# Kernel optimization log

Hardware: AMD Instinct MI355X
Metric: run time of the kernel (lower is better)

Reference implementation:

```python
import jax, jax.numpy as jnp
import numpy as np

N = 4096
D = 256
DEG = 32
E0 = N * DEG
RATIO = 0.5
NEG_SLOPE = 0.2


def setup_inputs() -> dict:
    key = jax.random.key(0)
    ks = jax.random.split(key, 12)
    # edges with NO self loops (so appending all N self-loops == add_remaining_self_loops)
    src = jax.random.randint(ks[0], (E0,), 0, N, dtype=jnp.int32)
    off = jax.random.randint(ks[1], (E0,), 1, N, dtype=jnp.int32)
    dst = ((src + off) % N).astype(jnp.int32)
    edge_index = jnp.stack([src, dst])
    edge_weight = jnp.ones((E0,), jnp.float32)
    x = jax.random.normal(ks[2], (N, D), jnp.float32)
    s = 1.0 / np.sqrt(D)
    u = lambda k, shp: jax.random.uniform(k, shp, jnp.float32, -s, s)
    return {
        'x': x,
        'edge_index': edge_index,
        'edge_weight': edge_weight,
        'lin_w': u(ks[3], (D, D)), 'lin_b': u(ks[4], (D,)),
        'att_w': jax.random.uniform(ks[5], (2 * D, 1), jnp.float32, -1.0 / np.sqrt(2 * D), 1.0 / np.sqrt(2 * D)),
        'att_b': u(ks[6], (1,)),
        'le1_w': u(ks[7], (D, 1)), 'le1_b': u(ks[8], (1,)),
        'le2_w': u(ks[9], (D, 1)),
        'le3_w': u(ks[10], (D, 1)), 'le3_b': u(ks[11], (1,)),
    }


def reference(x, edge_index, edge_weight, lin_w, lin_b, att_w, att_b,
              le1_w, le1_b, le2_w, le3_w, le3_b):
    n, d = x.shape
    # add_remaining_self_loops (input has no self loops by construction)
    loop = jnp.arange(n, dtype=edge_index.dtype)
    src = jnp.concatenate([edge_index[0], loop])
    dst = jnp.concatenate([edge_index[1], loop])
    w = jnp.concatenate([edge_weight, jnp.ones((n,), edge_weight.dtype)])

    # GNN is None -> x_pool = x
    x_pool_j = x[src]                                        # [E, D] gather
    x_q = jax.ops.segment_max(x_pool_j, dst, num_segments=n)  # scatter-max
    x_q_e = (x_q @ lin_w + lin_b)[dst]                        # [E, D]
    # att(cat([x_q, x_pool_j])) without materializing [E, 2D]
    score = x_q_e @ att_w[:d, 0] + x_pool_j @ att_w[d:, 0] + att_b[0]
    score = jax.nn.leaky_relu(score, NEG_SLOPE)
    # segment softmax over destination nodes
    smax = jax.ops.segment_max(score, dst, num_segments=n)
    ex = jnp.exp(score - smax[dst])
    denom = jax.ops.segment_sum(ex, dst, num_segments=n)
    score = ex / denom[dst]
    # dropout p=0 -> no-op
    xn = jax.ops.segment_sum(x_pool_j * score[:, None], dst, num_segments=n)

    # LEConv fitness: sigmoid( lin3(x) + sum_j (lin1(x_j) - lin2(x_i)) )
    a = xn @ le1_w + le1_b          # [N, 1]
    b = xn @ le2_w                  # [N, 1] (no bias)
    agg = jax.ops.segment_sum(a[src] - b[dst], dst, num_segments=n)
    fitness = jax.nn.sigmoid((agg + xn @ le3_w + le3_b)[:, 0])

    k = int(np.ceil(RATIO * N))
    _, perm = jax.lax.top_k(fitness, k)
    x_out = xn[perm] * fitness[perm][:, None]

    # Coarsening A_c = S[:, perm]^T @ A @ S[:, perm]; dense since SpGEMM nnz is data-dependent
    S = jnp.zeros((n, n), x.dtype).at[src, dst].add(score)[:, perm]  # [N, k]
    A = jnp.zeros((n, n), x.dtype).at[src, dst].add(w)               # [N, N]
    A_c = S.T @ (A @ S)                                              # [k, k]
    A_c = A_c * (1.0 - jnp.eye(k, dtype=A_c.dtype))                  # remove_diag
    return x_out, A_c, perm
```

## Files before the change

kernel.cpp:

```cpp
#include <hip/hip_runtime.h>
#include <cstdint>
#include <cstddef>
#include <math.h>

#define NN   4096
#define DD   256
#define E0S  131072
#define NE   (E0S + NN)
#define KK   2048
#define NEG_SLOPE 0.2f
#define SEGCAP 256

typedef float floatx4 __attribute__((ext_vector_type(4)));

__device__ __forceinline__ int esrc(const int* s, int e){ return e < E0S ? s[e] : e - E0S; }
__device__ __forceinline__ int edst(const int* d, int e){ return e < E0S ? d[e] : e - E0S; }

__global__ void init_kernel(int* deg_dst, int* deg_src, int* colmap, float* Ac, int zero_ac){
    int i = blockIdx.x * blockDim.x + threadIdx.x;
    int stride = gridDim.x * blockDim.x;
    if (zero_ac){
        for (size_t t = i; t < (size_t)KK * KK; t += stride) Ac[t] = 0.f;
    }
    for (int t = i; t < NN; t += stride){ deg_dst[t] = 0; deg_src[t] = 0; colmap[t] = -1; }
}

__global__ void count_kernel(const int* e_src, const int* e_dst, int* deg_dst, int* deg_src){
    int e = blockIdx.x * blockDim.x + threadIdx.x;
    if (e < NE){
        atomicAdd(&deg_dst[edst(e_dst, e)], 1);
        atomicAdd(&deg_src[esrc(e_src, e)], 1);
    }
}

__global__ void __launch_bounds__(1024) scan_kernel(const int* degA, int* offA, int* curA,
                                                    const int* degB, int* offB, int* curB){
    const int* deg = (blockIdx.x == 0) ? degA : degB;
    int* off = (blockIdx.x == 0) ? offA : offB;
    int* cur = (blockIdx.x == 0) ? curA : curB;
    __shared__ int part[1024];
    int t = threadIdx.x;
    int base = t * 4;
    int s0 = deg[base], s1 = deg[base+1], s2 = deg[base+2], s3 = deg[base+3];
    int tot = s0 + s1 + s2 + s3;
    part[t] = tot;
    __syncthreads();
    for (int d = 1; d < 1024; d <<= 1){
        int v = (t >= d) ? part[t - d] : 0;
        __syncthreads();
        part[t] += v;
        __syncthreads();
    }
    int excl = part[t] - tot;
    off[base]   = excl;            cur[base]   = excl;
    off[base+1] = excl + s0;       cur[base+1] = excl + s0;
    off[base+2] = excl + s0 + s1;  cur[base+2] = excl + s0 + s1;
    off[base+3] = excl + s0 + s1 + s2; cur[base+3] = excl + s0 + s1 + s2;
    if (t == 1023) off[NN] = part[1023];
}

__global__ void fill_kernel(const int* e_src, const int* e_dst, int* cur_dst, int* cur_src,
                            int* eid_dst, int* eid_src){
    int e = blockIdx.x * blockDim.x + threadIdx.x;
    if (e < NE){
        int p = atomicAdd(&cur_dst[edst(e_dst, e)], 1); eid_dst[p] = e;
        int q = atomicAdd(&cur_src[esrc(e_src, e)], 1); eid_src[q] = e;
    }
}

__global__ void segsort_kernel(const int* off_dst, int* eid_dst, const int* off_src, int* eid_src,
                               const int* e_src, int* isd){
    __shared__ int buf[4][SEGCAP];
    int wid  = (blockIdx.x * blockDim.x + threadIdx.x) >> 6;
    int lane = threadIdx.x & 63;
    int w    = threadIdx.x >> 6;
    const int* off; int* eid; int n; bool isdst;
    if (wid < NN){ off = off_dst; eid = eid_dst; n = wid; isdst = true; }
    else         { off = off_src; eid = eid_src; n = wid - NN; isdst = false; }
    int lo = off[n], hi = off[n+1];
    int L = hi - lo;
    int Lc = (L <= SEGCAP) ? L : SEGCAP;
    for (int i = lane; i < Lc; i += 64) buf[w][i] = eid[lo + i];
    __syncthreads();
    if (L <= SEGCAP){
        for (int i = lane; i < L; i += 64){
            int v = buf[w][i];
            int r = 0;
            for (int j = 0; j < L; ++j) r += (buf[w][j] < v);
            eid[lo + r] = v;
            if (isdst) isd[lo + r] = esrc(e_src, v);
        }
    } else if (lane == 0){
        for (int i = lo + 1; i < hi; ++i){
            int v = eid[i]; int j = i - 1;
            while (j >= lo && eid[j] > v){ eid[j+1] = eid[j]; --j; }
            eid[j+1] = v;
        }
        if (isdst) for (int i = lo; i < hi; ++i) isd[i] = esrc(e_src, eid[i]);
    }
}

__global__ void segmax_kernel(const float* x, const int* off, const int* isd, float* x_q){
    __shared__ int is_[SEGCAP];
    int n = blockIdx.x, d = threadIdx.x;
    int lo = off[n], hi = off[n+1];
    int L = hi - lo;
    int Ls = (L <= SEGCAP) ? L : SEGCAP;
    for (int t = d; t < Ls; t += 256) is_[t] = isd[lo + t];
    __syncthreads();
    float m = -INFINITY;
    int t = 0;
    for (; t + 1 < Ls; t += 2){
        float v0 = x[(size_t)is_[t]   * DD + d];
        float v1 = x[(size_t)is_[t+1] * DD + d];
        m = fmaxf(m, fmaxf(v0, v1));
    }
    if (t < Ls) m = fmaxf(m, x[(size_t)is_[t] * DD + d]);
    for (t = Ls; t < L; ++t)
        m = fmaxf(m, x[(size_t)isd[lo + t] * DD + d]);
    x_q[(size_t)n * DD + d] = m;
}

#define LROWS 8
__global__ void lin_kernel(const float* x_q, const float* w, const float* b, float* out){
    __shared__ float xs[LROWS][DD];
    int col = threadIdx.x;
    int r0 = blockIdx.x * LROWS;
    for (int r = 0; r < LROWS; ++r) xs[r][col] = x_q[(size_t)(r0 + r) * DD + col];
    __syncthreads();
    float acc[LROWS];
    float bc = b[col];
    #pragma unroll
    for (int r = 0; r < LROWS; ++r) acc[r] = bc;
    for (int kk = 0; kk < DD; ++kk){
        float wv = w[(size_t)kk * DD + col];
        #pragma unroll
        for (int r = 0; r < LROWS; ++r) acc[r] = fmaf(xs[r][kk], wv, acc[r]);
    }
    for (int r = 0; r < LROWS; ++r) out[(size_t)(r0 + r) * DD + col] = acc[r];
}

__global__ void nodedots_kernel(const float* x, const float* x_q_lin, const float* att_w,
                                float* q_s, float* p_s){
    int n = blockIdx.x, t = threadIdx.x;
    float v1 = x_q_lin[(size_t)n * DD + t] * att_w[t];
    float v2 = x[(size_t)n * DD + t] * att_w[DD + t];
    __shared__ float s1[256], s2[256];
    s1[t] = v1; s2[t] = v2;
    __syncthreads();
    for (int d = 128; d > 0; d >>= 1){
        if (t < d){ s1[t] += s1[t + d]; s2[t] += s2[t + d]; }
        __syncthreads();
    }
    if (t == 0){ q_s[n] = s1[0]; p_s[n] = s2[0]; }
}

__global__ void softmax_kernel(const int* off, const int* eid, const int* isd,
                               const float* q_s, const float* p_s, const float* att_b,
                               float* sc, float* ssd){
    int wave = threadIdx.x >> 6;
    int lane = threadIdx.x & 63;
    int n = blockIdx.x * 4 + wave;
    int lo = off[n], hi = off[n+1];
    float ab = att_b[0];
    float qn = q_s[n];
    float m = -INFINITY;
    for (int t = lo + lane; t < hi; t += 64){
        float s = qn + p_s[isd[t]] + ab;
        s = (s > 0.f) ? s : NEG_SLOPE * s;
        m = fmaxf(m, s);
    }
    #pragma unroll
    for (int d = 32; d > 0; d >>= 1) m = fmaxf(m, __shfl_xor(m, d));
    float sum = 0.f;
    for (int t = lo + lane; t < hi; t += 64){
        float s = qn + p_s[isd[t]] + ab;
        s = (s > 0.f) ? s : NEG_SLOPE * s;
        float ex = expf(s - m);
        ssd[t] = ex;
        sum += ex;
    }
    #pragma unroll
    for (int d = 32; d > 0; d >>= 1) sum += __shfl_xor(sum, d);
    float inv = 1.f / sum;
    for (int t = lo + lane; t < hi; t += 64){
        float v = ssd[t] * inv;
        ssd[t] = v;
        sc[eid[t]] = v;
    }
}

__global__ void xnfit_kernel(const float* x, const int* off, const int* isd, const float* ssd,
                             const float* le1_w, const float* le1_b, const float* le2_w,
                             const float* le3_w, const float* le3_b,
                             float* xn, float* a_, float* b_, float* c_){
    __shared__ int   is_[SEGCAP];
    __shared__ float ss_[SEGCAP];
    __shared__ float s1[256], s2[256], s3[256];
    int n = blockIdx.x, d = threadIdx.x;
    int lo = off[n], hi = off[n+1];
    int L = hi - lo;
    int Ls = (L <= SEGCAP) ? L : SEGCAP;
    for (int t = d; t < Ls; t += 256){
        is_[t] = isd[lo + t];
        ss_[t] = ssd[lo + t];
    }
    __syncthreads();
    float acc = 0.f;
    int t = 0;
    for (; t + 1 < Ls; t += 2){
        float v0 = x[(size_t)is_[t]   * DD + d];
        float v1 = x[(size_t)is_[t+1] * DD + d];
        acc = fmaf(ss_[t],   v0, acc);
        acc = fmaf(ss_[t+1], v1, acc);
    }
    if (t < Ls) acc = fmaf(ss_[t], x[(size_t)is_[t] * DD + d], acc);
    for (t = Ls; t < L; ++t)
        acc = fmaf(ssd[lo + t], x[(size_t)isd[lo + t] * DD + d], acc);
    xn[(size_t)n * DD + d] = acc;
    s1[d] = acc * le1_w[d];
    s2[d] = acc * le2_w[d];
    s3[d] = acc * le3_w[d];
    __syncthreads();
    for (int dd = 128; dd > 0; dd >>= 1){
        if (d < dd){ s1[d] += s1[d+dd]; s2[d] += s2[d+dd]; s3[d] += s3[d+dd]; }
        __syncthreads();
    }
    if (d == 0){
        a_[n] = s1[0] + le1_b[0];
        b_[n] = s2[0];
        c_[n] = s3[0] + le3_b[0];
    }
}

__global__ void fitness_kernel(const int* off, const int* isd,
                               const float* a_, const float* b_, const float* c_,
                               float* fit){
    int wave = threadIdx.x >> 6;
    int lane = threadIdx.x & 63;
    int n = blockIdx.x * 4 + wave;
    int lo = off[n], hi = off[n+1];
    float bn = b_[n];
    float s = 0.f;
    for (int t = lo + lane; t < hi; t += 64){
        s += a_[isd[t]] - bn;
    }
    #pragma unroll
    for (int d = 32; d > 0; d >>= 1) s += __shfl_xor(s, d);
    if (lane == 0){
        float z = s + c_[n];
        fit[n] = 1.f / (1.f + expf(-z));
    }
}

__global__ void __launch_bounds__(1024) topk_kernel(const float* fit, int* perm, int* colmap,
                                                    float* out_perm){
    __shared__ unsigned long long keys[NN];
    int t = threadIdx.x;
    for (int i = t; i < NN; i += 1024){
        unsigned int u = __float_as_uint(fit[i]);
        u = (u & 0x80000000u) ? ~u : (u | 0x80000000u);
        u = ~u;
        keys[i] = ((unsigned long long)u << 32) | (unsigned int)i;
    }
    __syncthreads();
    for (unsigned int ssize = 2; ssize <= NN; ssize <<= 1){
        for (unsigned int stride = ssize >> 1; stride > 0; stride >>= 1){
            for (int i = t; i < NN / 2; i += 1024){
                unsigned int idx = 2u * i - (i & (stride - 1u));
                unsigned int par = idx + stride;
                bool asc = ((idx & ssize) == 0u);
                unsigned long long a = keys[idx], b = keys[par];
                if ((a > b) == asc){ keys[idx] = b; keys[par] = a; }
            }
            __syncthreads();
        }
    }
    for (int i = t; i < KK; i += 1024){
        int node = (int)(keys[i] & 0xFFFFFFFFull);
        perm[i] = node;
        colmap[node] = i;
        out_perm[i] = (float)node;
    }
}

__global__ void xout_kernel(const float* xn, const float* fit, const int* perm, float* x_out){
    int r = blockIdx.x, d = threadIdx.x;
    int p = perm[r];
    x_out[(size_t)r * DD + d] = xn[(size_t)p * DD + d] * fit[p];
}

__global__ void prepsrc_kernel(const int* eid_src, const int* e_dst, const int* colmap,
                               const float* sc, int* cp, float* sp){
    int u = blockIdx.x * blockDim.x + threadIdx.x;
    if (u < NE){
        int f = eid_src[u];
        cp[u] = colmap[edst(e_dst, f)];
        sp[u] = sc[f];
    }
}

__global__ void spgemm1_kernel(const int* e_dst, const float* ew,
                               const int* off_src, const int* eid_src,
                               const int* cp, const float* sp, float* T){
    __shared__ float row[KK];
    __shared__ int   jlo_[SEGCAP];
    __shared__ int   jhi_[SEGCAP];
    __shared__ float w_[SEGCAP];
    int i = blockIdx.x;
    for (int c = threadIdx.x; c < KK; c += 256) row[c] = 0.f;
    int lo = off_src[i], hi = off_src[i+1];
    int L = hi - lo;
    int Ls = (L <= SEGCAP) ? L : SEGCAP;
    for (int t = threadIdx.x; t < Ls; t += 256){
        int e = eid_src[lo + t];
        int j = edst(e_dst, e);
        jlo_[t] = off_src[j];
        jhi_[t] = off_src[j+1];
        w_[t]   = (e < E0S) ? ew[e] : 1.0f;
    }
    __syncthreads();
    int wave = threadIdx.x >> 6, lane = threadIdx.x & 63;
    for (int t = wave; t < Ls; t += 4){
        float w1 = w_[t];
        for (int u = jlo_[t] + lane; u < jhi_[t]; u += 64){
            int c = cp[u];
            if (c >= 0) atomicAdd(&row[c], w1 * sp[u]);
        }
    }
    for (int t = Ls + wave; t < L; t += 4){
        int e = eid_src[lo + t];
        int j = edst(e_dst, e);
        float w1 = (e < E0S) ? ew[e] : 1.0f;
        int jlo = off_src[j], jhi = off_src[j+1];
        for (int u = jlo + lane; u < jhi; u += 64){
            int c = cp[u];
            if (c >= 0) atomicAdd(&row[c], w1 * sp[u]);
        }
    }
    __syncthreads();
    float* Trow = T + (size_t)i * KK;
    for (int c = threadIdx.x; c < KK; c += 256) Trow[c] = row[c];
}

__global__ void spgemm2_kernel(const int* perm, const int* off_dst,
                               const int* isd, const float* ssd,
                               const float* T, float* Ac){
    __shared__ int   is_[8][SEGCAP];
    __shared__ float ss_[8][SEGCAP];
    int bx = blockIdx.x;
    int by = blockIdx.y;
    int half = by >> 8;
    int rr   = by & 255;
    int sub  = threadIdx.x >> 5;
    int lane = threadIdx.x & 31;
    int r = rr * 8 + sub;
    int chunk = bx + 8 * half;
    int c0 = chunk * 128 + lane * 4;
    int node = perm[r];
    int lo = off_dst[node], hi = off_dst[node+1];
    int L = hi - lo;
    int Ls = (L <= SEGCAP) ? L : SEGCAP;
    for (int t = lane; t < Ls; t += 32){
        is_[sub][t] = isd[lo + t];
        ss_[sub][t] = ssd[lo + t];
    }
    __syncthreads();
    floatx4 acc = {0.f, 0.f, 0.f, 0.f};
    int t = 0;
    for (; t + 1 < Ls; t += 2){
        floatx4 a = *(const floatx4*)&T[(size_t)is_[sub][t]   * KK + c0];
        floatx4 b = *(const floatx4*)&T[(size_t)is_[sub][t+1] * KK + c0];
        float s0 = ss_[sub][t], s1 = ss_[sub][t+1];
        acc.x = fmaf(s0, a.x, acc.x); acc.y = fmaf(s0, a.y, acc.y);
        acc.z = fmaf(s0, a.z, acc.z); acc.w = fmaf(s0, a.w, acc.w);
        acc.x = fmaf(s1, b.x, acc.x); acc.y = fmaf(s1, b.y, acc.y);
        acc.z = fmaf(s1, b.z, acc.z); acc.w = fmaf(s1, b.w, acc.w);
    }
    for (; t < Ls; ++t){
        floatx4 a = *(const floatx4*)&T[(size_t)is_[sub][t] * KK + c0];
        float s0 = ss_[sub][t];
        acc.x = fmaf(s0, a.x, acc.x); acc.y = fmaf(s0, a.y, acc.y);
        acc.z = fmaf(s0, a.z, acc.z); acc.w = fmaf(s0, a.w, acc.w);
    }
    for (t = Ls; t < L; ++t){
        floatx4 a = *(const floatx4*)&T[(size_t)isd[lo + t] * KK + c0];
        float s0 = ssd[lo + t];
        acc.x = fmaf(s0, a.x, acc.x); acc.y = fmaf(s0, a.y, acc.y);
        acc.z = fmaf(s0, a.z, acc.z); acc.w = fmaf(s0, a.w, acc.w);
    }
    if (r - c0 >= 0 && r - c0 < 4){
        if (r - c0 == 0) acc.x = 0.f;
        else if (r - c0 == 1) acc.y = 0.f;
        else if (r - c0 == 2) acc.z = 0.f;
        else acc.w = 0.f;
    }
    __builtin_nontemporal_store(acc, (floatx4*)&Ac[(size_t)r * KK + c0]);
}

__global__ void ac_kernel(const int* e_src, const int* e_dst, const float* ew,
                          const int* off_src,
                          const int* cp, const float* sp, float* Ac){
    int e1 = blockIdx.x * blockDim.x + threadIdx.x;
    if (e1 >= NE) return;
    int i = (e1 < E0S) ? e_src[e1] : e1 - E0S;
    int j = (e1 < E0S) ? e_dst[e1] : e1 - E0S;
    float w1 = (e1 < E0S) ? ew[e1] : 1.0f;
    int ilo = off_src[i], ihi = off_src[i+1];
    int jlo = off_src[j], jhi = off_src[j+1];
    for (int ta = ilo; ta < ihi; ++ta){
        int ca = cp[ta];
        if (ca < 0) continue;
        float va = sp[ta] * w1;
        float* rowp = Ac + (size_t)ca * KK;
        for (int tb = jlo; tb < jhi; ++tb){
            int cb = cp[tb];
            if (cb < 0) continue;
            atomicAdd(&rowp[cb], va * sp[tb]);
        }
    }
}

__global__ void diag_kernel(float* Ac){
    int r = blockIdx.x * blockDim.x + threadIdx.x;
    if (r < KK) Ac[(size_t)r * KK + r] = 0.f;
}

extern "C" void kernel_launch(void* const* d_in, const int* in_sizes, int n_in,
                              void* d_out, int out_size, void* d_ws, size_t ws_size,
                              hipStream_t stream){
    const float* x     = (const float*)d_in[0];
    const int*   ei    = (const int*)d_in[1];
    const float* ew    = (const float*)d_in[2];
    const float* lin_w = (const float*)d_in[3];
    const float* lin_b = (const float*)d_in[4];
    const float* att_w = (const float*)d_in[5];
    const float* att_b = (const float*)d_in[6];
    const float* le1_w = (const float*)d_in[7];
    const float* le1_b = (const float*)d_in[8];
    const float* le2_w = (const float*)d_in[9];
    const float* le3_w = (const float*)d_in[10];
    const float* le3_b = (const float*)d_in[11];

    const int* e_src = ei;
    const int* e_dst = ei + E0S;

    float* out    = (float*)d_out;
    float* x_out  = out;
    float* Ac     = out + (size_t)KK * DD;
    float* operm  = out + (size_t)KK * DD + (size_t)KK * KK;

    char* wp = (char*)d_ws;
    auto alloc_i = [&](size_t n){ int* p = (int*)wp; wp += n * sizeof(int); return p; };
    auto alloc_f = [&](size_t n){ float* p = (float*)wp; wp += n * sizeof(float); return p; };

    int* deg_dst = alloc_i(NN);
    int* deg_src = alloc_i(NN);
    int* off_dst = alloc_i(NN + 1);
    int* off_src = alloc_i(NN + 1);
    int* cur_dst = alloc_i(NN);
    int* cur_src = alloc_i(NN);
    int* eid_dst = alloc_i(NE);
    int* eid_src = alloc_i(NE);
    int* colmap  = alloc_i(NN);
    int* perm    = alloc_i(KK);
    int* isd     = alloc_i(NE);
    int* cp      = alloc_i(NE);
    float* sp    = alloc_f(NE);
    float* ssd   = alloc_f(NE);
    float* q_s   = alloc_f(NN);
    float* p_s   = alloc_f(NN);
    float* a_    = alloc_f(NN);
    float* b_    = alloc_f(NN);
    float* c_    = alloc_f(NN);
    float* fit   = alloc_f(NN);
    float* sc    = alloc_f(NE);
    float* x_q   = alloc_f((size_t)NN * DD);
    float* x_ql  = alloc_f((size_t)NN * DD);
    float* xn    = alloc_f((size_t)NN * DD);
    float* T     = alloc_f((size_t)NN * KK);
    bool dense_ok = ((size_t)(wp - (char*)d_ws) <= ws_size);
    (void)n_in; (void)in_sizes; (void)out_size;

    const int EB = (NE + 255) / 256;

    init_kernel<<<2048, 256, 0, stream>>>(deg_dst, deg_src, colmap, Ac, dense_ok ? 0 : 1);
    count_kernel<<<EB, 256, 0, stream>>>(e_src, e_dst, deg_dst, deg_src);
    scan_kernel<<<2, 1024, 0, stream>>>(deg_dst, off_dst, cur_dst, deg_src, off_src, cur_src);
    fill_kernel<<<EB, 256, 0, stream>>>(e_src, e_dst, cur_dst, cur_src, eid_dst, eid_src);
    segsort_kernel<<<(2 * NN) / 4, 256, 0, stream>>>(off_dst, eid_dst, off_src, eid_src, e_src, isd);
    segmax_kernel<<<NN, 256, 0, stream>>>(x, off_dst, isd, x_q);
    lin_kernel<<<NN / LROWS, 256, 0, stream>>>(x_q, lin_w, lin_b, x_ql);
    nodedots_kernel<<<NN, 256, 0, stream>>>(x, x_ql, att_w, q_s, p_s);
    softmax_kernel<<<NN / 4, 256, 0, stream>>>(off_dst, eid_dst, isd, q_s, p_s, att_b, sc, ssd);
    xnfit_kernel<<<NN, 256, 0, stream>>>(x, off_dst, isd, ssd, le1_w, le1_b, le2_w, le3_w, le3_b,
                                         xn, a_, b_, c_);
    fitness_kernel<<<NN / 4, 256, 0, stream>>>(off_dst, isd, a_, b_, c_, fit);
    topk_kernel<<<1, 1024, 0, stream>>>(fit, perm, colmap, operm);
    xout_kernel<<<KK, 256, 0, stream>>>(xn, fit, perm, x_out);
    prepsrc_kernel<<<EB, 256, 0, stream>>>(eid_src, e_dst, colmap, sc, cp, sp);
    if (dense_ok){
        spgemm1_kernel<<<NN, 256, 0, stream>>>(e_dst, ew, off_src, eid_src, cp, sp, T);
        spgemm2_kernel<<<dim3(8, 512), 256, 0, stream>>>(perm, off_dst, isd, ssd, T, Ac);
    } else {
        ac_kernel<<<EB, 256, 0, stream>>>(e_src, e_dst, ew, off_src, cp, sp, Ac);
        diag_kernel<<<(KK + 255) / 256, 256, 0, stream>>>(Ac);
    }
}
```

Before: 228.4 us.

## Fuse segmax/linear/attention-dots, softmax/aggregation, and xout/prep kernels; narrow spgemm1 subgroups

Segment-max, the linear layer and the attention node dots now run in one kernel per 8-node block, so the x_q and x_ql intermediates are no longer written to or read from global memory. The segment softmax is folded into the xn aggregation kernel and keeps the softmax weights in shared memory. xout and prepsrc are merged into a single launch, and spgemm1 uses 32-lane subgroups in place of full waves for its inner scatter. Together these remove four launches and some global traffic. The trade-off is that the fused segmax stage has only 512 blocks, each looping serially over 8 nodes, which lowers parallelism for the gather-heavy work, and only one wave per block does the softmax while the others wait.

```diff
diff --git a/kernel.cpp b/kernel.cpp
--- a/kernel.cpp
+++ b/kernel.cpp
@@ -100,133 +100,129 @@
     }
 }
 
-__global__ void segmax_kernel(const float* x, const int* off, const int* isd, float* x_q){
-    __shared__ int is_[SEGCAP];
-    int n = blockIdx.x, d = threadIdx.x;
+#define LROWS 8
+__global__ void sml_kernel(const float* x, const int* off, const int* isd,
+                           const float* lin_w, const float* lin_b, const float* att_w,
+                           float* q_s, float* p_s){
+    __shared__ float xs[LROWS][DD];
+    __shared__ int   is_[SEGCAP];
+    __shared__ float s1[256], s2[256];
+    int col = threadIdx.x;
+    int r0 = blockIdx.x * LROWS;
+    for (int r = 0; r < LROWS; ++r){
+        int n = r0 + r;
+        int lo = off[n], hi = off[n+1];
+        int L = hi - lo;
+        int Ls = (L <= SEGCAP) ? L : SEGCAP;
+        for (int t = col; t < Ls; t += 256) is_[t] = isd[lo + t];
+        __syncthreads();
+        float m = -INFINITY;
+        int t = 0;
+        for (; t + 1 < Ls; t += 2){
+            float v0 = x[(size_t)is_[t]   * DD + col];
+            float v1 = x[(size_t)is_[t+1] * DD + col];
+            m = fmaxf(m, fmaxf(v0, v1));
+        }
+        if (t < Ls) m = fmaxf(m, x[(size_t)is_[t] * DD + col]);
+        for (t = Ls; t < L; ++t)
+            m = fmaxf(m, x[(size_t)isd[lo + t] * DD + col]);
+        xs[r][col] = m;
+        __syncthreads();
+    }
+    float acc[LROWS];
+    float bc = lin_b[col];
+    #pragma unroll
+    for (int r = 0; r < LROWS; ++r) acc[r] = bc;
+    for (int kk = 0; kk < DD; ++kk){
+        float wv = lin_w[(size_t)kk * DD + col];
+        #pragma unroll
+        for (int r = 0; r < LROWS; ++r) acc[r] = fmaf(xs[r][kk], wv, acc[r]);
+    }
+    float aw1 = att_w[col];
+    float aw2 = att_w[DD + col];
+    for (int r = 0; r < LROWS; ++r){
+        int n = r0 + r;
+        s1[col] = acc[r] * aw1;
+        s2[col] = x[(size_t)n * DD + col] * aw2;
+        __syncthreads();
+        for (int d = 128; d > 0; d >>= 1){
+            if (col < d){ s1[col] += s1[col + d]; s2[col] += s2[col + d]; }
+            __syncthreads();
+        }
+        if (col == 0){ q_s[n] = s1[0]; p_s[n] = s2[0]; }
+        __syncthreads();
+    }
+}
+
+__global__ void softxn_kernel(const float* x, const int* off, const int* eid, const int* isd,
+                              const float* q_s, const float* p_s, const float* att_b,
+                              const float* le1_w, const float* le1_b, const float* le2_w,
+                              const float* le3_w, const float* le3_b,
+                              float* sc, float* ssd, float* xn,
+                              float* a_, float* b_, float* c_){
+    __shared__ int   is_[SEGCAP];
+    __shared__ float ss_[SEGCAP];
+    __shared__ float s1[256], s2[256], s3[256];
+    int n = blockIdx.x, col = threadIdx.x;
     int lo = off[n], hi = off[n+1];
     int L = hi - lo;
     int Ls = (L <= SEGCAP) ? L : SEGCAP;
-    for (int t = d; t < Ls; t += 256) is_[t] = isd[lo + t];
-    __syncthreads();
-    float m = -INFINITY;
-    int t = 0;
-    for (; t + 1 < Ls; t += 2){
-        float v0 = x[(size_t)is_[t]   * DD + d];
-        float v1 = x[(size_t)is_[t+1] * DD + d];
-        m = fmaxf(m, fmaxf(v0, v1));
-    }
-    if (t < Ls) m = fmaxf(m, x[(size_t)is_[t] * DD + d]);
-    for (t = Ls; t < L; ++t)
-        m = fmaxf(m, x[(size_t)isd[lo + t] * DD + d]);
-    x_q[(size_t)n * DD + d] = m;
-}
-
-#define LROWS 8
-__global__ void lin_kernel(const float* x_q, const float* w, const float* b, float* out){
-    __shared__ float xs[LROWS][DD];
-    int col = threadIdx.x;
-    int r0 = blockIdx.x * LROWS;
-    for (int r = 0; r < LROWS; ++r) xs[r][col] = x_q[(size_t)(r0 + r) * DD + col];
-    __syncthreads();
-    float acc[LROWS];
-    float bc = b[col];
-    #pragma unroll
-    for (int r = 0; r < LROWS; ++r) acc[r] = bc;
-    for (int kk = 0; kk < DD; ++kk){
-        float wv = w[(size_t)kk * DD + col];
+    for (int t = col; t < Ls; t += 256) is_[t] = isd[lo + t];
+    __syncthreads();
+    if (col < 64){
+        int lane = col;
+        float ab = att_b[0];
+        float qn = q_s[n];
+        float m = -INFINITY;
+        for (int t = lane; t < L; t += 64){
+            int sn = (t < Ls) ? is_[t] : isd[lo + t];
+            float s = qn + p_s[sn] + ab;
+            s = (s > 0.f) ? s : NEG_SLOPE * s;
+            m = fmaxf(m, s);
+        }
         #pragma unroll
-        for (int r = 0; r < LROWS; ++r) acc[r] = fmaf(xs[r][kk], wv, acc[r]);
-    }
-    for (int r = 0; r < LROWS; ++r) out[(size_t)(r0 + r) * DD + col] = acc[r];
-}
-
-__global__ void nodedots_kernel(const float* x, const float* x_q_lin, const float* att_w,
-                                float* q_s, float* p_s){
-    int n = blockIdx.x, t = threadIdx.x;
-    float v1 = x_q_lin[(size_t)n * DD + t] * att_w[t];
-    float v2 = x[(size_t)n * DD + t] * att_w[DD + t];
-    __shared__ float s1[256], s2[256];
-    s1[t] = v1; s2[t] = v2;
-    __syncthreads();
-    for (int d = 128; d > 0; d >>= 1){
-        if (t < d){ s1[t] += s1[t + d]; s2[t] += s2[t + d]; }
-        __syncthreads();
-    }
-    if (t == 0){ q_s[n] = s1[0]; p_s[n] = s2[0]; }
-}
-
-__global__ void softmax_kernel(const int* off, const int* eid, const int* isd,
-                               const float* q_s, const float* p_s, const float* att_b,
-                               float* sc, float* ssd){
-    int wave = threadIdx.x >> 6;
-    int lane = threadIdx.x & 63;
-    int n = blockIdx.x * 4 + wave;
-    int lo = off[n], hi = off[n+1];
-    float ab = att_b[0];
-    float qn = q_s[n];
-    float m = -INFINITY;
-    for (int t = lo + lane; t < hi; t += 64){
-        float s = qn + p_s[isd[t]] + ab;
-        s = (s > 0.f) ? s : NEG_SLOPE * s;
-        m = fmaxf(m, s);
-    }
-    #pragma unroll
-    for (int d = 32; d > 0; d >>= 1) m = fmaxf(m, __shfl_xor(m, d));
-    float sum = 0.f;
-    for (int t = lo + lane; t < hi; t += 64){
-        float s = qn + p_s[isd[t]] + ab;
-        s = (s > 0.f) ? s : NEG_SLOPE * s;
-        float ex = expf(s - m);
-        ssd[t] = ex;
-        sum += ex;
-    }
-    #pragma unroll
-    for (int d = 32; d > 0; d >>= 1) sum += __shfl_xor(sum, d);
-    float inv = 1.f / sum;
-    for (int t = lo + lane; t < hi; t += 64){
-        float v = ssd[t] * inv;
-        ssd[t] = v;
-        sc[eid[t]] = v;
-    }
-}
-
-__global__ void xnfit_kernel(const float* x, const int* off, const int* isd, const float* ssd,
-                             const float* le1_w, const float* le1_b, const float* le2_w,
-                             const float* le3_w, const float* le3_b,
-                             float* xn, float* a_, float* b_, float* c_){
-    __shared__ int   is_[SEGCAP];
-    __shared__ float ss_[SEGCAP];
-    __shared__ float s1[256], s2[256], s3[256];
-    int n = blockIdx.x, d = threadIdx.x;
-    int lo = off[n], hi = off[n+1];
-    int L = hi - lo;
-    int Ls = (L <= SEGCAP) ? L : SEGCAP;
-    for (int t = d; t < Ls; t += 256){
-        is_[t] = isd[lo + t];
-        ss_[t] = ssd[lo + t];
+        for (int d = 32; d > 0; d >>= 1) m = fmaxf(m, __shfl_xor(m, d));
+        float sum = 0.f;
+        for (int t = lane; t < L; t += 64){
+            int sn = (t < Ls) ? is_[t] : isd[lo + t];
+            float s = qn + p_s[sn] + ab;
+            s = (s > 0.f) ? s : NEG_SLOPE * s;
+            float ex = expf(s - m);
+            if (t < Ls) ss_[t] = ex; else ssd[lo + t] = ex;
+            sum += ex;
+        }
+        #pragma unroll
+        for (int d = 32; d > 0; d >>= 1) sum += __shfl_xor(sum, d);
+        float inv = 1.f / sum;
+        for (int t = lane; t < L; t += 64){
+            float v = ((t < Ls) ? ss_[t] : ssd[lo + t]) * inv;
+            if (t < Ls) ss_[t] = v;
+            ssd[lo + t] = v;
+            sc[eid[lo + t]] = v;
+        }
     }
     __syncthreads();
     float acc = 0.f;
     int t = 0;
     for (; t + 1 < Ls; t += 2){
-        float v0 = x[(size_t)is_[t]   * DD + d];
-        float v1 = x[(size_t)is_[t+1] * DD + d];
+        float v0 = x[(size_t)is_[t]   * DD + col];
+        float v1 = x[(size_t)is_[t+1] * DD + col];
         acc = fmaf(ss_[t],   v0, acc);
         acc = fmaf(ss_[t+1], v1, acc);
     }
-    if (t < Ls) acc = fmaf(ss_[t], x[(size_t)is_[t] * DD + d], acc);
+    if (t < Ls) acc = fmaf(ss_[t], x[(size_t)is_[t] * DD + col], acc);
     for (t = Ls; t < L; ++t)
-        acc = fmaf(ssd[lo + t], x[(size_t)isd[lo + t] * DD + d], acc);
-    xn[(size_t)n * DD + d] = acc;
-    s1[d] = acc * le1_w[d];
-    s2[d] = acc * le2_w[d];
-    s3[d] = acc * le3_w[d];
+        acc = fmaf(ssd[lo + t], x[(size_t)isd[lo + t] * DD + col], acc);
+    xn[(size_t)n * DD + col] = acc;
+    s1[col] = acc * le1_w[col];
+    s2[col] = acc * le2_w[col];
+    s3[col] = acc * le3_w[col];
     __syncthreads();
     for (int dd = 128; dd > 0; dd >>= 1){
-        if (d < dd){ s1[d] += s1[d+dd]; s2[d] += s2[d+dd]; s3[d] += s3[d+dd]; }
-        __syncthreads();
-    }
-    if (d == 0){
+        if (col < dd){ s1[col] += s1[col+dd]; s2[col] += s2[col+dd]; s3[col] += s3[col+dd]; }
+        __syncthreads();
+    }
+    if (col == 0){
         a_[n] = s1[0] + le1_b[0];
         b_[n] = s2[0];
         c_[n] = s3[0] + le3_b[0];
@@ -284,19 +280,21 @@
     }
 }
 
-__global__ void xout_kernel(const float* xn, const float* fit, const int* perm, float* x_out){
-    int r = blockIdx.x, d = threadIdx.x;
-    int p = perm[r];
-    x_out[(size_t)r * DD + d] = xn[(size_t)p * DD + d] * fit[p];
-}
-
-__global__ void prepsrc_kernel(const int* eid_src, const int* e_dst, const int* colmap,
-                               const float* sc, int* cp, float* sp){
-    int u = blockIdx.x * blockDim.x + threadIdx.x;
-    if (u < NE){
-        int f = eid_src[u];
-        cp[u] = colmap[edst(e_dst, f)];
-        sp[u] = sc[f];
+__global__ void xoutprep_kernel(const float* xn, const float* fit, const int* perm, float* x_out,
+                                const int* eid_src, const int* e_dst, const int* colmap,
+                                const float* sc, int* cp, float* sp){
+    int b = blockIdx.x;
+    if (b < KK){
+        int r = b, d = threadIdx.x;
+        int p = perm[r];
+        x_out[(size_t)r * DD + d] = xn[(size_t)p * DD + d] * fit[p];
+    } else {
+        int u = (b - KK) * 256 + threadIdx.x;
+        if (u < NE){
+            int f = eid_src[u];
+            cp[u] = colmap[edst(e_dst, f)];
+            sp[u] = sc[f];
+        }
     }
 }
 
@@ -320,20 +318,20 @@
         w_[t]   = (e < E0S) ? ew[e] : 1.0f;
     }
     __syncthreads();
-    int wave = threadIdx.x >> 6, lane = threadIdx.x & 63;
-    for (int t = wave; t < Ls; t += 4){
+    int sw = threadIdx.x >> 5, ln = threadIdx.x & 31;
+    for (int t = sw; t < Ls; t += 8){
         float w1 = w_[t];
-        for (int u = jlo_[t] + lane; u < jhi_[t]; u += 64){
+        for (int u = jlo_[t] + ln; u < jhi_[t]; u += 32){
             int c = cp[u];
             if (c >= 0) atomicAdd(&row[c], w1 * sp[u]);
         }
     }
-    for (int t = Ls + wave; t < L; t += 4){
+    for (int t = Ls + sw; t < L; t += 8){
         int e = eid_src[lo + t];
         int j = edst(e_dst, e);
         float w1 = (e < E0S) ? ew[e] : 1.0f;
         int jlo = off_src[j], jhi = off_src[j+1];
-        for (int u = jlo + lane; u < jhi; u += 64){
+        for (int u = jlo + ln; u < jhi; u += 32){
             int c = cp[u];
             if (c >= 0) atomicAdd(&row[c], w1 * sp[u]);
         }
@@ -475,8 +473,6 @@
     float* c_    = alloc_f(NN);
     float* fit   = alloc_f(NN);
     float* sc    = alloc_f(NE);
-    float* x_q   = alloc_f((size_t)NN * DD);
-    float* x_ql  = alloc_f((size_t)NN * DD);
     float* xn    = alloc_f((size_t)NN * DD);
     float* T     = alloc_f((size_t)NN * KK);
     bool dense_ok = ((size_t)(wp - (char*)d_ws) <= ws_size);
@@ -489,16 +485,14 @@
     scan_kernel<<<2, 1024, 0, stream>>>(deg_dst, off_dst, cur_dst, deg_src, off_src, cur_src);
     fill_kernel<<<EB, 256, 0, stream>>>(e_src, e_dst, cur_dst, cur_src, eid_dst, eid_src);
     segsort_kernel<<<(2 * NN) / 4, 256, 0, stream>>>(off_dst, eid_dst, off_src, eid_src, e_src, isd);
-    segmax_kernel<<<NN, 256, 0, stream>>>(x, off_dst, isd, x_q);
-    lin_kernel<<<NN / LROWS, 256, 0, stream>>>(x_q, lin_w, lin_b, x_ql);
-    nodedots_kernel<<<NN, 256, 0, stream>>>(x, x_ql, att_w, q_s, p_s);
-    softmax_kernel<<<NN / 4, 256, 0, stream>>>(off_dst, eid_dst, isd, q_s, p_s, att_b, sc, ssd);
-    xnfit_kernel<<<NN, 256, 0, stream>>>(x, off_dst, isd, ssd, le1_w, le1_b, le2_w, le3_w, le3_b,
-                                         xn, a_, b_, c_);
+    sml_kernel<<<NN / LROWS, 256, 0, stream>>>(x, off_dst, isd, lin_w, lin_b, att_w, q_s, p_s);
+    softxn_kernel<<<NN, 256, 0, stream>>>(x, off_dst, eid_dst, isd, q_s, p_s, att_b,
+                                          le1_w, le1_b, le2_w, le3_w, le3_b,
+                                          sc, ssd, xn, a_, b_, c_);
     fitness_kernel<<<NN / 4, 256, 0, stream>>>(off_dst, isd, a_, b_, c_, fit);
     topk_kernel<<<1, 1024, 0, stream>>>(fit, perm, colmap, operm);
-    xout_kernel<<<KK, 256, 0, stream>>>(xn, fit, perm, x_out);
-    prepsrc_kernel<<<EB, 256, 0, stream>>>(eid_src, e_dst, colmap, sc, cp, sp);
+    xoutprep_kernel<<<KK + EB, 256, 0, stream>>>(xn, fit, perm, x_out,
+                                                 eid_src, e_dst, colmap, sc, cp, sp);
     if (dense_ok){
         spgemm1_kernel<<<NN, 256, 0, stream>>>(e_dst, ew, off_src, eid_src, cp, sp, T);
         spgemm2_kernel<<<dim3(8, 512), 256, 0, stream>>>(perm, off_dst, isd, ssd, T, Ac);
```

After: 231.6 us. Within noise of the previous version (+1.4%).
